# Optimization experiments

Measured on AMD Instinct MI355X. Metric: run time of the kernel, lower is better.

## Reference

```python
import jax, jax.numpy as jnp
import numpy as np

NEG_SLOPE = 0.2  # GAT LeakyReLU slope
EPS = 1e-16


def _pagat_conv(x, path_index, W, a, b, heads, out_ch, concat):
    """Path-augmented GAT conv: attention over (head, mid, tail) path triples,
    messages flow tail -> head, softmax-normalized per destination node."""
    N = x.shape[0]
    head, mid, tail = path_index[0], path_index[1], path_index[2]
    h = (x @ W).reshape(N, heads, out_ch)            # [N, H, C]
    # attention logits from all three path positions: [P, H]
    e = (jnp.einsum('phc,hc->ph', h[head], a[0])
         + jnp.einsum('phc,hc->ph', h[mid], a[1])
         + jnp.einsum('phc,hc->ph', h[tail], a[2]))
    e = jax.nn.leaky_relu(e, NEG_SLOPE)
    # segment softmax over paths grouped by destination (head) node
    m = jax.ops.segment_max(e, head, num_segments=N)  # [N, H]
    ex = jnp.exp(e - m[head])
    s = jax.ops.segment_sum(ex, head, num_segments=N)  # [N, H]
    alpha = ex / (s[head] + EPS)                       # [P, H]
    # aggregate tail features weighted by attention
    out = jax.ops.segment_sum(alpha[..., None] * h[tail], head, num_segments=N)  # [N, H, C]
    if concat:
        out = out.reshape(N, heads * out_ch)
    else:
        out = out.mean(axis=1)
    return out + b


def setup_inputs() -> dict:
    key = jax.random.key(0)
    ks = jax.random.split(key, 8)
    N, F_in, H, C, CLS, P = 100000, 500, 8, 16, 16, 1000000
    x = jax.random.normal(ks[0], (N, F_in), dtype=jnp.float32)
    path_index = jax.random.randint(ks[1], (3, P), 0, N, dtype=jnp.int32)
    W1 = jax.random.normal(ks[2], (F_in, H * C), dtype=jnp.float32) * 0.05
    a1 = jax.random.normal(ks[3], (3, H, C), dtype=jnp.float32) * 0.05
    b1 = jnp.zeros((H * C,), dtype=jnp.float32)
    W2 = jax.random.normal(ks[4], (H * C, CLS), dtype=jnp.float32) * 0.05
    a2 = jax.random.normal(ks[5], (3, 1, CLS), dtype=jnp.float32) * 0.05
    b2 = jnp.zeros((CLS,), dtype=jnp.float32)
    return {"x": x, "path_index": path_index, "W1": W1, "a1": a1, "b1": b1,
            "W2": W2, "a2": a2, "b2": b2}


def reference(x, path_index, W1, a1, b1, W2, a2, b2):
    # eval mode: dropout is identity
    h = _pagat_conv(x, path_index, W1, a1, b1, heads=8, out_ch=16, concat=True)
    h = jax.nn.elu(h)
    h = _pagat_conv(h, path_index, W2, a2, b2, heads=1, out_ch=16, concat=False)
    return jax.nn.log_softmax(h, axis=1)
```

## Files before the change

kernel.cpp:

```cpp
#include <hip/hip_runtime.h>
#include <hip/hip_bf16.h>

#define F_IN  500
#define HC    128
#define NHEAD 8
#define CDIM  16
#define NCLS  16
#define KPAD  512

static __device__ __forceinline__ float bf(const __hip_bfloat16 v) {
    return __bfloat162float(v);
}

static __device__ __forceinline__ unsigned int enc_f32(float f) {
    unsigned int u = __float_as_uint(f);
    return (u & 0x80000000u) ? ~u : (u | 0x80000000u);
}
static __device__ __forceinline__ float dec_f32(unsigned int u) {
    return __uint_as_float((u & 0x80000000u) ? (u & 0x7FFFFFFFu) : ~u);
}

typedef __bf16 bf16x8 __attribute__((ext_vector_type(8)));
typedef float f32x4 __attribute__((ext_vector_type(4)));

__global__ void zero_i32(int* __restrict__ p, int n) {
    int i = blockIdx.x * blockDim.x + threadIdx.x;
    if (i < n) p[i] = 0;
}

__global__ void transpose_w1(const float* __restrict__ W1,
                             __bf16* __restrict__ w1t_hi,
                             __bf16* __restrict__ w1t_lo)
{
    int id = blockIdx.x * 256 + threadIdx.x;
    int c = id >> 9, k = id & 511;
    float v = (k < F_IN) ? W1[k * HC + c] : 0.f;
    __bf16 h = (__bf16)v;
    w1t_hi[id] = h;
    w1t_lo[id] = (__bf16)(v - (float)h);
}

static __device__ __forceinline__ void split8(const float4 a, const float4 b,
                                              bf16x8& hi, bf16x8& lo) {
    float v[8] = {a.x, a.y, a.z, a.w, b.x, b.y, b.z, b.w};
#pragma unroll
    for (int j = 0; j < 8; j++) {
        __bf16 h = (__bf16)v[j];
        hi[j] = h;
        lo[j] = (__bf16)(v[j] - (float)h);
    }
}

__global__ __launch_bounds__(256) void gemm1_mfma(
    const float* __restrict__ x,
    const __bf16* __restrict__ w1t_hi, const __bf16* __restrict__ w1t_lo,
    __hip_bfloat16* __restrict__ h1, int N)
{
    const int wave = threadIdx.x >> 6, lane = threadIdx.x & 63;
    const int m = lane & 15, q = lane >> 4;
    const int row0 = blockIdx.x * 128 + wave * 32;

    long ra0 = row0 + m, ra1 = row0 + 16 + m;
    if (ra0 >= N) ra0 = 0;
    if (ra1 >= N) ra1 = 0;
    const float* pa0 = x + ra0 * F_IN + q * 8;
    const float* pa1 = x + ra1 * F_IN + q * 8;
    const __bf16* pbh = w1t_hi + (size_t)m * KPAD + q * 8;
    const __bf16* pbl = w1t_lo + (size_t)m * KPAD + q * 8;

    f32x4 acc[2][8];
#pragma unroll
    for (int i = 0; i < 2; i++)
#pragma unroll
        for (int t = 0; t < 8; t++) acc[i][t] = (f32x4){0.f, 0.f, 0.f, 0.f};

#pragma unroll
    for (int k0 = 0; k0 < 480; k0 += 32) {
        bf16x8 a0h, a0l, a1h, a1l;
        split8(*(const float4*)(pa0 + k0), *(const float4*)(pa0 + k0 + 4), a0h, a0l);
        split8(*(const float4*)(pa1 + k0), *(const float4*)(pa1 + k0 + 4), a1h, a1l);
#pragma unroll
        for (int t = 0; t < 8; t++) {
            bf16x8 bh = *(const bf16x8*)(pbh + t * 16 * KPAD + k0);
            bf16x8 bl = *(const bf16x8*)(pbl + t * 16 * KPAD + k0);
            acc[0][t] = __builtin_amdgcn_mfma_f32_16x16x32_bf16(a0h, bh, acc[0][t], 0, 0, 0);
            acc[0][t] = __builtin_amdgcn_mfma_f32_16x16x32_bf16(a0h, bl, acc[0][t], 0, 0, 0);
            acc[0][t] = __builtin_amdgcn_mfma_f32_16x16x32_bf16(a0l, bh, acc[0][t], 0, 0, 0);
            acc[1][t] = __builtin_amdgcn_mfma_f32_16x16x32_bf16(a1h, bh, acc[1][t], 0, 0, 0);
            acc[1][t] = __builtin_amdgcn_mfma_f32_16x16x32_bf16(a1h, bl, acc[1][t], 0, 0, 0);
            acc[1][t] = __builtin_amdgcn_mfma_f32_16x16x32_bf16(a1l, bh, acc[1][t], 0, 0, 0);
        }
    }
    {
        const float4 z4 = make_float4(0.f, 0.f, 0.f, 0.f);
        bf16x8 a0h, a0l, a1h, a1l;
        float4 u0 = (q < 3) ? *(const float4*)(pa0 + 480) : z4;
        float4 u1 = (q < 2) ? *(const float4*)(pa0 + 484) : z4;
        float4 w0 = (q < 3) ? *(const float4*)(pa1 + 480) : z4;
        float4 w1 = (q < 2) ? *(const float4*)(pa1 + 484) : z4;
        split8(u0, u1, a0h, a0l);
        split8(w0, w1, a1h, a1l);
#pragma unroll
        for (int t = 0; t < 8; t++) {
            bf16x8 bh = *(const bf16x8*)(pbh + t * 16 * KPAD + 480);
            bf16x8 bl = *(const bf16x8*)(pbl + t * 16 * KPAD + 480);
            acc[0][t] = __builtin_amdgcn_mfma_f32_16x16x32_bf16(a0h, bh, acc[0][t], 0, 0, 0);
            acc[0][t] = __builtin_amdgcn_mfma_f32_16x16x32_bf16(a0h, bl, acc[0][t], 0, 0, 0);
            acc[0][t] = __builtin_amdgcn_mfma_f32_16x16x32_bf16(a0l, bh, acc[0][t], 0, 0, 0);
            acc[1][t] = __builtin_amdgcn_mfma_f32_16x16x32_bf16(a1h, bh, acc[1][t], 0, 0, 0);
            acc[1][t] = __builtin_amdgcn_mfma_f32_16x16x32_bf16(a1h, bl, acc[1][t], 0, 0, 0);
            acc[1][t] = __builtin_amdgcn_mfma_f32_16x16x32_bf16(a1l, bh, acc[1][t], 0, 0, 0);
        }
    }
#pragma unroll
    for (int rt = 0; rt < 2; rt++) {
        int rbase = row0 + rt * 16 + q * 4;
#pragma unroll
        for (int t = 0; t < 8; t++) {
#pragma unroll
            for (int r = 0; r < 4; r++) {
                int row = rbase + r;
                if (row < N)
                    h1[(size_t)row * HC + t * 16 + m] = __float2bfloat16(acc[rt][t][r]);
            }
        }
    }
}

__global__ void dots1_kernel(const __hip_bfloat16* __restrict__ h1,
                             const float* __restrict__ a1,
                             float* __restrict__ d1, int N)
{
    int id = blockIdx.x * blockDim.x + threadIdx.x;
    if (id >= N * NHEAD) return;
    int n = id >> 3, h = id & 7;
    const __hip_bfloat16* hp = h1 + (size_t)n * HC + h * CDIM;
    float s0 = 0.f, s1 = 0.f, s2 = 0.f;
#pragma unroll
    for (int c = 0; c < CDIM; c++) {
        float v = bf(hp[c]);
        s0 += v * a1[(0 * NHEAD + h) * CDIM + c];
        s1 += v * a1[(1 * NHEAD + h) * CDIM + c];
        s2 += v * a1[(2 * NHEAD + h) * CDIM + c];
    }
    d1[id] = s0;
    d1[N * NHEAD + id] = s1;
    d1[2 * N * NHEAD + id] = s2;
}

__global__ void maxred_d1(const float* __restrict__ d1,
                          unsigned int* __restrict__ gmax, int N)
{
    __shared__ unsigned int sm[16];
    if (threadIdx.x < 16) sm[threadIdx.x] = 0;
    __syncthreads();
    int total = 2 * N * NHEAD;
    for (int i = blockIdx.x * blockDim.x + threadIdx.x; i < total;
         i += gridDim.x * blockDim.x) {
        float v = d1[(size_t)N * NHEAD + i];
        int slot = ((i >= N * NHEAD) ? 8 : 0) + (i & 7);
        atomicMax(&sm[slot], enc_f32(v));
    }
    __syncthreads();
    if (threadIdx.x < 16) atomicMax(&gmax[threadIdx.x], sm[threadIdx.x]);
}

__global__ void maxred_d2(const float* __restrict__ d2,
                          unsigned int* __restrict__ gmax2, int N)
{
    __shared__ unsigned int sm[2];
    if (threadIdx.x < 2) sm[threadIdx.x] = 0;
    __syncthreads();
    int total = 2 * N;
    for (int i = blockIdx.x * blockDim.x + threadIdx.x; i < total;
         i += gridDim.x * blockDim.x) {
        float v = d2[N + i];
        atomicMax(&sm[i >= N ? 1 : 0], enc_f32(v));
    }
    __syncthreads();
    if (threadIdx.x < 2) atomicMax(&gmax2[threadIdx.x], sm[threadIdx.x]);
}

__global__ void hist_kernel(const int* __restrict__ pidx, int* __restrict__ deg, int P) {
    int p = blockIdx.x * blockDim.x + threadIdx.x;
    if (p < P) atomicAdd(deg + pidx[p], 1);
}

__global__ void scan1_kernel(const int* __restrict__ deg, int* __restrict__ start,
                             int* __restrict__ bsum, int N) {
    __shared__ int sh[256];
    int i = blockIdx.x * 256 + threadIdx.x;
    int v = (i < N) ? deg[i] : 0;
    sh[threadIdx.x] = v;
    __syncthreads();
#pragma unroll
    for (int off = 1; off < 256; off <<= 1) {
        int x = (threadIdx.x >= off) ? sh[threadIdx.x - off] : 0;
        __syncthreads();
        sh[threadIdx.x] += x;
        __syncthreads();
    }
    if (i < N) start[i] = sh[threadIdx.x] - v;
    if (threadIdx.x == 255) bsum[blockIdx.x] = sh[255];
}

__global__ void scan2_kernel(int* __restrict__ bsum, int nb) {
    __shared__ int sh[512];
    int v = (threadIdx.x < nb) ? bsum[threadIdx.x] : 0;
    sh[threadIdx.x] = v;
    __syncthreads();
#pragma unroll
    for (int off = 1; off < 512; off <<= 1) {
        int x = (threadIdx.x >= off) ? sh[threadIdx.x - off] : 0;
        __syncthreads();
        sh[threadIdx.x] += x;
        __syncthreads();
    }
    if (threadIdx.x < nb) bsum[threadIdx.x] = sh[threadIdx.x] - v;
}

__global__ void scan3_kernel(int* __restrict__ start, const int* __restrict__ bsum, int N) {
    int i = blockIdx.x * 256 + threadIdx.x;
    if (i < N) start[i] += bsum[blockIdx.x];
}

__global__ void scatter_kernel(const int* __restrict__ pidx,
                               const int* __restrict__ start,
                               int* __restrict__ cursor,
                               int* __restrict__ csr, int P) {
    int p = blockIdx.x * blockDim.x + threadIdx.x;
    if (p >= P) return;
    int hd = pidx[p];
    int pos = atomicAdd(cursor + hd, 1);
    csr[start[hd] + pos] = p;
}

__global__ __launch_bounds__(256) void attn1_csr_kernel(
    const int* __restrict__ csr, const int* __restrict__ start,
    const int* __restrict__ deg, const int* __restrict__ pidx,
    const float* __restrict__ d1, const __hip_bfloat16* __restrict__ h1,
    const float* __restrict__ b1, const unsigned int* __restrict__ gmax,
    float* __restrict__ elu_out, int N, int P)
{
    int node = blockIdx.x * 4 + (threadIdx.x >> 6);
    if (node >= N) return;
    int lane = threadIdx.x & 63;
    int h = lane >> 3;
    int s0 = start[node], dg = deg[node];
    const float* d1m = d1 + (size_t)N * NHEAD;
    const float* d1t = d1 + (size_t)2 * N * NHEAD;
    const float dh = d1[node * NHEAD + h];
    float zub = dh + dec_f32(gmax[h]) + dec_f32(gmax[8 + h]);
    const float mxub = zub > 0.f ? zub : 0.2f * zub;

    float acc0 = 0.f, acc1 = 0.f, den = 0.f;
    for (int k0 = 0; k0 < dg; k0 += 8) {
        int kk = k0 + (lane & 7);
        bool valid = kk < dg;
        int p = csr[s0 + (valid ? kk : dg - 1)];
        int mid = pidx[P + p], tl = pidx[2 * P + p];
        float z = dh + d1m[mid * NHEAD + h] + d1t[tl * NHEAD + h];
        float e = z > 0.f ? z : 0.2f * z;
        float ex = valid ? __expf(e - mxub) : 0.f;
        den += ex;
        int kmax = dg - k0; if (kmax > 8) kmax = 8;
        for (int dk = 0; dk < kmax; dk++) {
            int tl_b = __shfl(tl, dk, 8);
            float ex_b = __shfl(ex, dk, 8);
            __hip_bfloat162 v = *(const __hip_bfloat162*)(h1 + (size_t)tl_b * HC + 2 * lane);
            acc0 += ex_b * bf(v.x);
            acc1 += ex_b * bf(v.y);
        }
    }
#pragma unroll
    for (int w = 1; w < 8; w <<= 1) den += __shfl_xor(den, w, 8);

    float inv = 1.f / (den + 1e-16f);
    int j0 = 2 * lane;
    float v0 = acc0 * inv + b1[j0];
    float v1 = acc1 * inv + b1[j0 + 1];
    v0 = v0 > 0.f ? v0 : __expf(v0) - 1.f;
    v1 = v1 > 0.f ? v1 : __expf(v1) - 1.f;
    *(float2*)(elu_out + (size_t)node * HC + j0) = make_float2(v0, v1);
}

__global__ __launch_bounds__(256) void layer2_kernel(
    const float* __restrict__ elu, const float* __restrict__ W2,
    const float* __restrict__ a2,
    float* __restrict__ h2, float* __restrict__ d2, int N)
{
    __shared__ float rows[16][HC + 1];
    __shared__ float h2s[16][NCLS + 1];
    const int n0 = blockIdx.x * 16;
    const int tid = threadIdx.x;
    for (int idx = tid; idx < 16 * HC; idx += 256) {
        int r = idx >> 7, c = idx & 127;
        rows[r][c] = (n0 + r < N) ? elu[(size_t)(n0 + r) * HC + c] : 0.f;
    }
    __syncthreads();
    int ln = tid >> 4, c = tid & 15;
    float acc = 0.f;
#pragma unroll 8
    for (int j = 0; j < HC; j++) acc += rows[ln][j] * W2[j * NCLS + c];
    h2s[ln][c] = acc;
    if (n0 + ln < N) h2[(size_t)(n0 + ln) * NCLS + c] = acc;
    __syncthreads();
    if (tid < 48) {
        int l = tid / 3, j = tid - l * 3;
        if (n0 + l < N) {
            float s = 0.f;
#pragma unroll
            for (int cc = 0; cc < NCLS; cc++) s += h2s[l][cc] * a2[j * NCLS + cc];
            d2[j * N + n0 + l] = s;
        }
    }
}

__global__ __launch_bounds__(256) void attn2_csr_kernel(
    const int* __restrict__ csr, const int* __restrict__ start,
    const int* __restrict__ deg, const int* __restrict__ pidx,
    const float* __restrict__ d2, const float* __restrict__ h2,
    const float* __restrict__ b2, const unsigned int* __restrict__ gmax2,
    float* __restrict__ out, int N, int P)
{
    int node = blockIdx.x * 16 + (threadIdx.x >> 4);
    if (node >= N) return;
    int c = threadIdx.x & 15;
    int s0 = start[node], dg = deg[node];
    const float dh = d2[node];
    const float* d2m = d2 + N;
    const float* d2t = d2 + 2 * N;
    float zub = dh + dec_f32(gmax2[0]) + dec_f32(gmax2[1]);
    const float mxub = zub > 0.f ? zub : 0.2f * zub;

    float acc = 0.f, den = 0.f;
    for (int k0 = 0; k0 < dg; k0 += 16) {
        int kk = k0 + c;
        bool valid = kk < dg;
        int p = csr[s0 + (valid ? kk : dg - 1)];
        int mid = pidx[P + p], tl = pidx[2 * P + p];
        float z = dh + d2m[mid] + d2t[tl];
        float e = z > 0.f ? z : 0.2f * z;
        float ex = valid ? __expf(e - mxub) : 0.f;
        den += ex;
        int kmax = dg - k0; if (kmax > 16) kmax = 16;
        for (int dk = 0; dk < kmax; dk++) {
            int tl_b = __shfl(tl, dk, 16);
            float ex_b = __shfl(ex, dk, 16);
            acc += ex_b * h2[(size_t)tl_b * NCLS + c];
        }
    }
#pragma unroll
    for (int w = 1; w < 16; w <<= 1) den += __shfl_xor(den, w, 16);

    float o = acc / (den + 1e-16f) + b2[c];
    float m2 = o;
#pragma unroll
    for (int w = 1; w < 16; w <<= 1) m2 = fmaxf(m2, __shfl_xor(m2, w, 16));
    float ex = __expf(o - m2), sm = ex;
#pragma unroll
    for (int w = 1; w < 16; w <<= 1) sm += __shfl_xor(sm, w, 16);
    float r = o - m2 - __logf(sm);
    out[(size_t)node * NCLS + c] = r;
}

extern "C" void kernel_launch(void* const* d_in, const int* in_sizes, int n_in,
                              void* d_out, int out_size, void* d_ws, size_t ws_size,
                              hipStream_t stream)
{
    const float* x  = (const float*)d_in[0];
    const int*   pi = (const int*)d_in[1];
    const float* W1 = (const float*)d_in[2];
    const float* a1 = (const float*)d_in[3];
    const float* b1 = (const float*)d_in[4];
    const float* W2 = (const float*)d_in[5];
    const float* a2 = (const float*)d_in[6];
    const float* b2 = (const float*)d_in[7];

    const int N = in_sizes[0] / F_IN;
    const int P = in_sizes[1] / 3;

    float* ws = (float*)d_ws;
    size_t off_h1     = 0;
    size_t off_d1     = (size_t)64 * N;
    size_t off_elu    = (size_t)88 * N;
    size_t off_h2     = (size_t)216 * N;
    size_t off_d2     = (size_t)232 * N;
    size_t off_deg    = (size_t)235 * N;
    size_t off_start  = (size_t)236 * N;
    size_t off_cursor = (size_t)237 * N;
    size_t off_gmax   = (size_t)238 * N;
    size_t off_bsum   = (size_t)238 * N + 32;
    size_t off_csr    = (size_t)238 * N + 32 + 1024;
    size_t off_w1th   = off_csr + P;
    size_t off_w1tl   = off_w1th + 32768;

    __hip_bfloat16* h1 = (__hip_bfloat16*)(ws + off_h1);
    float* d1   = ws + off_d1;
    float* elu  = ws + off_elu;
    float* h2   = ws + off_h2;
    float* d2   = ws + off_d2;
    int* deg    = (int*)(ws + off_deg);
    int* start  = (int*)(ws + off_start);
    int* cursor = (int*)(ws + off_cursor);
    unsigned int* gmax  = (unsigned int*)(ws + off_gmax);
    unsigned int* gmax2 = (unsigned int*)(ws + off_gmax) + 16;
    int* bsum   = (int*)(ws + off_bsum);
    int* csr    = (int*)(ws + off_csr);
    __bf16* w1t_hi = (__bf16*)(ws + off_w1th);
    __bf16* w1t_lo = (__bf16*)(ws + off_w1tl);

    const int BLK = 256;
    const int nb = (N + 255) / 256;

    transpose_w1<<<(HC * KPAD) / 256, 256, 0, stream>>>(W1, w1t_hi, w1t_lo);
    zero_i32<<<(3 * N + 32 + BLK - 1) / BLK, BLK, 0, stream>>>(deg, 3 * N + 32);
    gemm1_mfma<<<(N + 127) / 128, 256, 0, stream>>>(x, w1t_hi, w1t_lo, h1, N);
    dots1_kernel<<<(N * NHEAD + BLK - 1) / BLK, BLK, 0, stream>>>(h1, a1, d1, N);
    maxred_d1<<<1024, 256, 0, stream>>>(d1, gmax, N);
    hist_kernel<<<(P + BLK - 1) / BLK, BLK, 0, stream>>>(pi, deg, P);
    scan1_kernel<<<nb, 256, 0, stream>>>(deg, start, bsum, N);
    scan2_kernel<<<1, 512, 0, stream>>>(bsum, nb);
    scan3_kernel<<<nb, 256, 0, stream>>>(start, bsum, N);
    scatter_kernel<<<(P + BLK - 1) / BLK, BLK, 0, stream>>>(pi, start, cursor, csr, P);
    attn1_csr_kernel<<<(N + 3) / 4, 256, 0, stream>>>(csr, start, deg, pi, d1, h1, b1, gmax, elu, N, P);
    layer2_kernel<<<(N + 15) / 16, 256, 0, stream>>>(elu, W2, a2, h2, d2, N);
    maxred_d2<<<256, 256, 0, stream>>>(d2, gmax2, N);
    attn2_csr_kernel<<<(N + 15) / 16, 256, 0, stream>>>(csr, start, deg, pi, d2, h2, b2, gmax2,
                                                        (float*)d_out, N, P);
}
```

Before: 747.9 us.

## Split GEMM1 output columns across waves instead of rows

Each block now handles 32 rows, and each of its four waves computes 32 of the 128 output columns, where before each wave computed all 128 columns for its own 32 rows. This cuts per-thread accumulator registers from 64 to 16 floats, which should raise occupancy, and gives four times as many blocks. The cost is that every wave in a block reloads the same x rows, so x traffic through cache grows by up to four times, though the loads may hit in L1/L2.

```diff
diff --git a/kernel.cpp b/kernel.cpp
--- a/kernel.cpp
+++ b/kernel.cpp
@@ -58,38 +58,45 @@
 {
     const int wave = threadIdx.x >> 6, lane = threadIdx.x & 63;
     const int m = lane & 15, q = lane >> 4;
-    const int row0 = blockIdx.x * 128 + wave * 32;
+    const int row0 = blockIdx.x * 32;
 
     long ra0 = row0 + m, ra1 = row0 + 16 + m;
     if (ra0 >= N) ra0 = 0;
     if (ra1 >= N) ra1 = 0;
     const float* pa0 = x + ra0 * F_IN + q * 8;
     const float* pa1 = x + ra1 * F_IN + q * 8;
-    const __bf16* pbh = w1t_hi + (size_t)m * KPAD + q * 8;
-    const __bf16* pbl = w1t_lo + (size_t)m * KPAD + q * 8;
-
-    f32x4 acc[2][8];
+    const __bf16* pbh0 = w1t_hi + (size_t)(2 * wave * 16 + m) * KPAD + q * 8;
+    const __bf16* pbl0 = w1t_lo + (size_t)(2 * wave * 16 + m) * KPAD + q * 8;
+    const __bf16* pbh1 = pbh0 + 16 * KPAD;
+    const __bf16* pbl1 = pbl0 + 16 * KPAD;
+
+    f32x4 acc[2][2];
 #pragma unroll
     for (int i = 0; i < 2; i++)
 #pragma unroll
-        for (int t = 0; t < 8; t++) acc[i][t] = (f32x4){0.f, 0.f, 0.f, 0.f};
+        for (int t = 0; t < 2; t++) acc[i][t] = (f32x4){0.f, 0.f, 0.f, 0.f};
 
 #pragma unroll
     for (int k0 = 0; k0 < 480; k0 += 32) {
         bf16x8 a0h, a0l, a1h, a1l;
         split8(*(const float4*)(pa0 + k0), *(const float4*)(pa0 + k0 + 4), a0h, a0l);
         split8(*(const float4*)(pa1 + k0), *(const float4*)(pa1 + k0 + 4), a1h, a1l);
-#pragma unroll
-        for (int t = 0; t < 8; t++) {
-            bf16x8 bh = *(const bf16x8*)(pbh + t * 16 * KPAD + k0);
-            bf16x8 bl = *(const bf16x8*)(pbl + t * 16 * KPAD + k0);
-            acc[0][t] = __builtin_amdgcn_mfma_f32_16x16x32_bf16(a0h, bh, acc[0][t], 0, 0, 0);
-            acc[0][t] = __builtin_amdgcn_mfma_f32_16x16x32_bf16(a0h, bl, acc[0][t], 0, 0, 0);
-            acc[0][t] = __builtin_amdgcn_mfma_f32_16x16x32_bf16(a0l, bh, acc[0][t], 0, 0, 0);
-            acc[1][t] = __builtin_amdgcn_mfma_f32_16x16x32_bf16(a1h, bh, acc[1][t], 0, 0, 0);
-            acc[1][t] = __builtin_amdgcn_mfma_f32_16x16x32_bf16(a1h, bl, acc[1][t], 0, 0, 0);
-            acc[1][t] = __builtin_amdgcn_mfma_f32_16x16x32_bf16(a1l, bh, acc[1][t], 0, 0, 0);
-        }
+        bf16x8 bh0 = *(const bf16x8*)(pbh0 + k0);
+        bf16x8 bl0 = *(const bf16x8*)(pbl0 + k0);
+        bf16x8 bh1 = *(const bf16x8*)(pbh1 + k0);
+        bf16x8 bl1 = *(const bf16x8*)(pbl1 + k0);
+        acc[0][0] = __builtin_amdgcn_mfma_f32_16x16x32_bf16(a0h, bh0, acc[0][0], 0, 0, 0);
+        acc[0][0] = __builtin_amdgcn_mfma_f32_16x16x32_bf16(a0h, bl0, acc[0][0], 0, 0, 0);
+        acc[0][0] = __builtin_amdgcn_mfma_f32_16x16x32_bf16(a0l, bh0, acc[0][0], 0, 0, 0);
+        acc[1][0] = __builtin_amdgcn_mfma_f32_16x16x32_bf16(a1h, bh0, acc[1][0], 0, 0, 0);
+        acc[1][0] = __builtin_amdgcn_mfma_f32_16x16x32_bf16(a1h, bl0, acc[1][0], 0, 0, 0);
+        acc[1][0] = __builtin_amdgcn_mfma_f32_16x16x32_bf16(a1l, bh0, acc[1][0], 0, 0, 0);
+        acc[0][1] = __builtin_amdgcn_mfma_f32_16x16x32_bf16(a0h, bh1, acc[0][1], 0, 0, 0);
+        acc[0][1] = __builtin_amdgcn_mfma_f32_16x16x32_bf16(a0h, bl1, acc[0][1], 0, 0, 0);
+        acc[0][1] = __builtin_amdgcn_mfma_f32_16x16x32_bf16(a0l, bh1, acc[0][1], 0, 0, 0);
+        acc[1][1] = __builtin_amdgcn_mfma_f32_16x16x32_bf16(a1h, bh1, acc[1][1], 0, 0, 0);
+        acc[1][1] = __builtin_amdgcn_mfma_f32_16x16x32_bf16(a1h, bl1, acc[1][1], 0, 0, 0);
+        acc[1][1] = __builtin_amdgcn_mfma_f32_16x16x32_bf16(a1l, bh1, acc[1][1], 0, 0, 0);
     }
     {
         const float4 z4 = make_float4(0.f, 0.f, 0.f, 0.f);
@@ -100,28 +107,34 @@
         float4 w1 = (q < 2) ? *(const float4*)(pa1 + 484) : z4;
         split8(u0, u1, a0h, a0l);
         split8(w0, w1, a1h, a1l);
-#pragma unroll
-        for (int t = 0; t < 8; t++) {
-            bf16x8 bh = *(const bf16x8*)(pbh + t * 16 * KPAD + 480);
-            bf16x8 bl = *(const bf16x8*)(pbl + t * 16 * KPAD + 480);
-            acc[0][t] = __builtin_amdgcn_mfma_f32_16x16x32_bf16(a0h, bh, acc[0][t], 0, 0, 0);
-            acc[0][t] = __builtin_amdgcn_mfma_f32_16x16x32_bf16(a0h, bl, acc[0][t], 0, 0, 0);
-            acc[0][t] = __builtin_amdgcn_mfma_f32_16x16x32_bf16(a0l, bh, acc[0][t], 0, 0, 0);
-            acc[1][t] = __builtin_amdgcn_mfma_f32_16x16x32_bf16(a1h, bh, acc[1][t], 0, 0, 0);
-            acc[1][t] = __builtin_amdgcn_mfma_f32_16x16x32_bf16(a1h, bl, acc[1][t], 0, 0, 0);
-            acc[1][t] = __builtin_amdgcn_mfma_f32_16x16x32_bf16(a1l, bh, acc[1][t], 0, 0, 0);
-        }
+        bf16x8 bh0 = *(const bf16x8*)(pbh0 + 480);
+        bf16x8 bl0 = *(const bf16x8*)(pbl0 + 480);
+        bf16x8 bh1 = *(const bf16x8*)(pbh1 + 480);
+        bf16x8 bl1 = *(const bf16x8*)(pbl1 + 480);
+        acc[0][0] = __builtin_amdgcn_mfma_f32_16x16x32_bf16(a0h, bh0, acc[0][0], 0, 0, 0);
+        acc[0][0] = __builtin_amdgcn_mfma_f32_16x16x32_bf16(a0h, bl0, acc[0][0], 0, 0, 0);
+        acc[0][0] = __builtin_amdgcn_mfma_f32_16x16x32_bf16(a0l, bh0, acc[0][0], 0, 0, 0);
+        acc[1][0] = __builtin_amdgcn_mfma_f32_16x16x32_bf16(a1h, bh0, acc[1][0], 0, 0, 0);
+        acc[1][0] = __builtin_amdgcn_mfma_f32_16x16x32_bf16(a1h, bl0, acc[1][0], 0, 0, 0);
+        acc[1][0] = __builtin_amdgcn_mfma_f32_16x16x32_bf16(a1l, bh0, acc[1][0], 0, 0, 0);
+        acc[0][1] = __builtin_amdgcn_mfma_f32_16x16x32_bf16(a0h, bh1, acc[0][1], 0, 0, 0);
+        acc[0][1] = __builtin_amdgcn_mfma_f32_16x16x32_bf16(a0h, bl1, acc[0][1], 0, 0, 0);
+        acc[0][1] = __builtin_amdgcn_mfma_f32_16x16x32_bf16(a0l, bh1, acc[0][1], 0, 0, 0);
+        acc[1][1] = __builtin_amdgcn_mfma_f32_16x16x32_bf16(a1h, bh1, acc[1][1], 0, 0, 0);
+        acc[1][1] = __builtin_amdgcn_mfma_f32_16x16x32_bf16(a1h, bl1, acc[1][1], 0, 0, 0);
+        acc[1][1] = __builtin_amdgcn_mfma_f32_16x16x32_bf16(a1l, bh1, acc[1][1], 0, 0, 0);
     }
 #pragma unroll
     for (int rt = 0; rt < 2; rt++) {
         int rbase = row0 + rt * 16 + q * 4;
 #pragma unroll
-        for (int t = 0; t < 8; t++) {
+        for (int tt = 0; tt < 2; tt++) {
+            int col = (2 * wave + tt) * 16 + m;
 #pragma unroll
             for (int r = 0; r < 4; r++) {
                 int row = rbase + r;
                 if (row < N)
-                    h1[(size_t)row * HC + t * 16 + m] = __float2bfloat16(acc[rt][t][r]);
+                    h1[(size_t)row * HC + col] = __float2bfloat16(acc[rt][tt][r]);
             }
         }
     }
@@ -415,7 +428,7 @@
 
     transpose_w1<<<(HC * KPAD) / 256, 256, 0, stream>>>(W1, w1t_hi, w1t_lo);
     zero_i32<<<(3 * N + 32 + BLK - 1) / BLK, BLK, 0, stream>>>(deg, 3 * N + 32);
-    gemm1_mfma<<<(N + 127) / 128, 256, 0, stream>>>(x, w1t_hi, w1t_lo, h1, N);
+    gemm1_mfma<<<(N + 31) / 32, 256, 0, stream>>>(x, w1t_hi, w1t_lo, h1, N);
     dots1_kernel<<<(N * NHEAD + BLK - 1) / BLK, BLK, 0, stream>>>(h1, a1, d1, N);
     maxred_d1<<<1024, 256, 0, stream>>>(d1, gmax, N);
     hist_kernel<<<(P + BLK - 1) / BLK, BLK, 0, stream>>>(pi, deg, P);
```

Measured after the change: 769.0 us. 1.03x slower.
